# Performance work log

Measured on AMD Instinct MI355X. Metric: run time of the kernel, lower is better.

Reference implementation:

```python
import jax, jax.numpy as jnp
import numpy as np

T, H, I, E = 512, 2048, 1408, 16
G, TOPK_GROUP, TOP_K = 4, 2, 6
RSF = 2.5  # routed_scaling_factor


def setup_inputs() -> dict:
    key = jax.random.key(0)
    ks = jax.random.split(key, 6)
    s = jnp.float32(0.02)
    return {
        "hidden_states": jax.random.normal(ks[0], (T, H), jnp.float32),
        "gate_weight": jax.random.normal(ks[1], (E, H), jnp.float32) * s,
        "correction_bias": jax.random.normal(ks[2], (E,), jnp.float32) * s,
        "w_gate": jax.random.normal(ks[3], (E, I, H), jnp.float32) * s,
        "w_up": jax.random.normal(ks[4], (E, I, H), jnp.float32) * s,
        "w_down": jax.random.normal(ks[5], (E, H, I), jnp.float32) * s,
    }


def _route(x, gate_weight, correction_bias):
    # MoEGate: logits = x @ W^T ; noaux_tc biased grouped top-k (sigmoid scoring)
    logits = x @ gate_weight.T                       # [T, E]
    scores = jax.nn.sigmoid(logits)                  # [T, E]
    sfc = scores + correction_bias                   # scores used for selection only
    # group score = sum of top-2 biased scores within each group
    gs = sfc.reshape(-1, G, E // G)                  # [T, G, E/G]
    group_scores = jax.lax.top_k(gs, 2)[0].sum(-1)   # [T, G]
    gidx = jax.lax.top_k(group_scores, TOPK_GROUP)[1]        # [T, topk_group]
    gmask = jnp.sum(jax.nn.one_hot(gidx, G, dtype=x.dtype), axis=1)  # [T, G]
    emask = jnp.repeat(gmask, E // G, axis=1)        # [T, E]
    masked = jnp.where(emask > 0, sfc, -jnp.inf)
    topk_idx = jax.lax.top_k(masked, TOP_K)[1]       # [T, K]
    # weights come from the UNbiased sigmoid scores
    topk_w = jnp.take_along_axis(scores, topk_idx, axis=1)   # [T, K]
    topk_w = topk_w / jnp.sum(topk_w, axis=-1, keepdims=True)  # renormalize
    topk_w = topk_w * jnp.asarray(RSF, x.dtype)      # routed_scaling_factor
    return topk_w, topk_idx


def _moe(x, topk_w, topk_idx, w_gate, w_up, w_down):
    # dispatch/grouped-GEMM/combine, expressed as a scan over experts with
    # per-token combine coefficients (same math as gather/grouped-GEMM/scatter)
    def step(acc, ws):
        wg, wu, wd, e = ws
        h = jax.nn.silu(x @ wg.T) * (x @ wu.T)       # [T, I] SiluAndMul
        out_e = h @ wd.T                             # [T, H]
        coef = jnp.sum(jnp.where(topk_idx == e, topk_w, 0.0), axis=1)  # [T]
        return acc + coef[:, None] * out_e, None

    acc0 = jnp.zeros_like(x)
    acc, _ = jax.lax.scan(step, acc0, (w_gate, w_up, w_down, jnp.arange(E)))
    return acc


def reference(hidden_states, gate_weight, correction_bias, w_gate, w_up, w_down):
    topk_w, topk_idx = _route(hidden_states, gate_weight, correction_bias)
    return _moe(hidden_states, topk_w, topk_idx, w_gate, w_up, w_down)
```

## Files before the change

kernel.cpp:

```cpp
#include <hip/hip_runtime.h>
#include <cstdint>

#define T_TOK 512
#define H_DIM 2048
#define I_DIM 1408
#define N_EXP 16

typedef __attribute__((ext_vector_type(8))) _Float16 f16x8;
typedef __attribute__((ext_vector_type(4))) float f32x4;

__device__ __forceinline__ void gload_lds16(const void* g, void* l) {
  auto gp = (const __attribute__((address_space(1))) unsigned int*)(unsigned long long)g;
  unsigned int loff = (unsigned int)(unsigned long long)l;
  auto lp = (__attribute__((address_space(3))) unsigned int*)loff;
  __builtin_amdgcn_global_load_lds(gp, lp, 16, 0, 0);
}

__device__ __forceinline__ f16x8 cvt8(f32x4 a, f32x4 b) {
  f16x8 r;
  r[0] = (_Float16)a[0]; r[1] = (_Float16)a[1]; r[2] = (_Float16)a[2]; r[3] = (_Float16)a[3];
  r[4] = (_Float16)b[0]; r[5] = (_Float16)b[1]; r[6] = (_Float16)b[2]; r[7] = (_Float16)b[3];
  return r;
}

__global__ __launch_bounds__(256) void route_kernel(
    const float* __restrict__ x, const float* __restrict__ gw,
    const float* __restrict__ bias, float* __restrict__ coef,
    _Float16* __restrict__ xb) {
  const int t = blockIdx.x;
  const int tid = threadIdx.x;
  const float* xt = x + (size_t)t * H_DIM;
  _Float16* xbt = xb + (size_t)t * H_DIM;

  float part[N_EXP];
#pragma unroll
  for (int e = 0; e < N_EXP; ++e) part[e] = 0.f;
  for (int j = tid; j < H_DIM; j += 256) {
    float xv = xt[j];
    xbt[j] = (_Float16)xv;
#pragma unroll
    for (int e = 0; e < N_EXP; ++e) part[e] += xv * gw[e * H_DIM + j];
  }
#pragma unroll
  for (int e = 0; e < N_EXP; ++e) {
#pragma unroll
    for (int off = 32; off > 0; off >>= 1) part[e] += __shfl_down(part[e], off);
  }
  __shared__ float red[4][N_EXP];
  const int lane = tid & 63, w = tid >> 6;
  if (lane == 0) {
#pragma unroll
    for (int e = 0; e < N_EXP; ++e) red[w][e] = part[e];
  }
  __syncthreads();
  if (tid == 0) {
    float s[16], sf[16];
    for (int e = 0; e < 16; ++e) {
      float lg = red[0][e] + red[1][e] + red[2][e] + red[3][e];
      s[e] = 1.f / (1.f + expf(-lg));
      sf[e] = s[e] + bias[e];
    }
    float gsc[4];
    for (int g = 0; g < 4; ++g) {
      float m1 = -1e30f, m2 = -1e30f;
      for (int j = 0; j < 4; ++j) {
        float v = sf[g * 4 + j];
        if (v > m1) { m2 = m1; m1 = v; }
        else if (v > m2) { m2 = v; }
      }
      gsc[g] = m1 + m2;
    }
    int g1 = 0;
    for (int g = 1; g < 4; ++g) if (gsc[g] > gsc[g1]) g1 = g;
    int g2 = -1;
    for (int g = 0; g < 4; ++g) {
      if (g == g1) continue;
      if (g2 < 0 || gsc[g] > gsc[g2]) g2 = g;
    }
    bool gok[4];
    for (int g = 0; g < 4; ++g) gok[g] = (g == g1) || (g == g2);
    bool sel[16];
    for (int e = 0; e < 16; ++e) sel[e] = false;
    float wsum = 0.f;
    for (int k = 0; k < 6; ++k) {
      int best = -1; float bv = 0.f;
      for (int e2 = 0; e2 < 16; ++e2) {
        if (!gok[e2 >> 2] || sel[e2]) continue;
        if (best < 0 || sf[e2] > bv) { bv = sf[e2]; best = e2; }
      }
      sel[best] = true;
      wsum += s[best];
    }
    float inv = 2.5f / wsum;
    for (int e = 0; e < 16; ++e) coef[t * N_EXP + e] = sel[e] ? s[e] * inv : 0.f;
  }
}

__global__ __launch_bounds__(512) void build_lists_kernel(
    const float* __restrict__ coef, int* __restrict__ counts,
    int* __restrict__ lists) {
  const int e = blockIdx.x;
  const int t = threadIdx.x;
  const bool flag = coef[t * N_EXP + e] != 0.f;
  const unsigned long long m = __ballot(flag);
  const int lane = t & 63, w = t >> 6;
  __shared__ int wcnt[8], woff[8];
  if (lane == 0) wcnt[w] = __popcll(m);
  __syncthreads();
  if (t == 0) {
    int a = 0;
    for (int i = 0; i < 8; ++i) { woff[i] = a; a += wcnt[i]; }
    counts[e] = a;
  }
  __syncthreads();
  if (flag) {
    int pos = woff[w] + __popcll(m & ((1ull << lane) - 1ull));
    lists[e * T_TOK + pos] = t;
  }
}

__global__ __launch_bounds__(256, 2) void gate_up_kernel(
    const _Float16* __restrict__ xb, const float* __restrict__ wg,
    const float* __restrict__ wu, const int* __restrict__ counts,
    const int* __restrict__ lists, _Float16* __restrict__ hbuf) {
  extern __shared__ char lds[];
  const int e = blockIdx.z;
  const int ne = counts[e];
  const int row0 = blockIdx.y * 256;
  if (row0 >= ne) return;
  const int col0 = blockIdx.x * 64;
  const int tid = threadIdx.x;
  const int lane = tid & 63;
  const int w = tid >> 6;

  const int* lst = lists + e * T_TOK;
  const _Float16* asrc[4];
#pragma unroll
  for (int i = 0; i < 4; ++i) {
    int r = row0 + (4 * w + i) * 16 + (lane & 15);
    int tok = lst[min(r, ne - 1)];
    asrc[i] = xb + (size_t)tok * H_DIM + (lane >> 4) * 8;
  }
  const float* bgs[2];
  const float* bus[2];
#pragma unroll
  for (int i = 0; i < 2; ++i) {
    int tr = (w * 2 + i) * 8 + (lane >> 3);
    int ls = (lane & 7) ^ (tr & 7);
    bgs[i] = wg + ((size_t)e * I_DIM + col0 + tr) * H_DIM + ls * 4;
    bus[i] = wu + ((size_t)e * I_DIM + col0 + tr) * H_DIM + ls * 4;
  }

  f32x4 accg[4][4], accu[4][4];
  const f32x4 zz = {0.f, 0.f, 0.f, 0.f};
#pragma unroll
  for (int m = 0; m < 4; ++m)
#pragma unroll
    for (int n = 0; n < 4; ++n) { accg[m][n] = zz; accu[m][n] = zz; }

  auto stage = [&](int kt, int buf) {
    const int k0 = kt * 32;
#pragma unroll
    for (int i = 0; i < 4; ++i)
      gload_lds16(asrc[i] + k0, lds + buf * 16384 + (4 * w + i) * 1024);
#pragma unroll
    for (int i = 0; i < 2; ++i) {
      gload_lds16(bgs[i] + k0, lds + 32768 + buf * 8192 + (w * 2 + i) * 1024);
      gload_lds16(bus[i] + k0, lds + 49152 + buf * 8192 + (w * 2 + i) * 1024);
    }
  };

  auto comp = [&](int buf) {
    const char* Ab = lds + buf * 16384;
    const char* Gb = lds + 32768 + buf * 8192;
    const char* Ub = lds + 49152 + buf * 8192;
    f16x8 afr[4];
#pragma unroll
    for (int m = 0; m < 4; ++m)
      afr[m] = *(const f16x8*)(Ab + (w * 4 + m) * 1024 + lane * 16);
    const int s0 = (lane >> 4) * 2;
#pragma unroll
    for (int n = 0; n < 4; ++n) {
      int c = n * 16 + (lane & 15);
      int p0 = s0 ^ (c & 7);
      int p1 = (s0 + 1) ^ (c & 7);
      f16x8 bg = cvt8(*(const f32x4*)(Gb + c * 128 + p0 * 16),
                      *(const f32x4*)(Gb + c * 128 + p1 * 16));
      f16x8 bu = cvt8(*(const f32x4*)(Ub + c * 128 + p0 * 16),
                      *(const f32x4*)(Ub + c * 128 + p1 * 16));
#pragma unroll
      for (int m = 0; m < 4; ++m) {
        accg[m][n] = __builtin_amdgcn_mfma_f32_16x16x32_f16(afr[m], bg, accg[m][n], 0, 0, 0);
        accu[m][n] = __builtin_amdgcn_mfma_f32_16x16x32_f16(afr[m], bu, accu[m][n], 0, 0, 0);
      }
    }
  };

  const int NK = H_DIM / 32;
  stage(0, 0);
  for (int kt = 0; kt < NK; ++kt) {
    __syncthreads();
    if (kt + 1 < NK) stage(kt + 1, (kt + 1) & 1);
    comp(kt & 1);
  }

  _Float16* hb = hbuf + (size_t)e * T_TOK * I_DIM;
#pragma unroll
  for (int m = 0; m < 4; ++m) {
#pragma unroll
    for (int j = 0; j < 4; ++j) {
      int r = row0 + w * 64 + m * 16 + (lane >> 4) * 4 + j;
      if (r < ne) {
#pragma unroll
        for (int n = 0; n < 4; ++n) {
          int cc = col0 + n * 16 + (lane & 15);
          float g = accg[m][n][j];
          float u = accu[m][n][j];
          float hv = (g / (1.f + __expf(-g))) * u;
          hb[(size_t)r * I_DIM + cc] = (_Float16)hv;
        }
      }
    }
  }
}

__global__ __launch_bounds__(512) void down_kernel(
    const _Float16* __restrict__ hbuf, const float* __restrict__ wd,
    const int* __restrict__ counts, const int* __restrict__ lists,
    const float* __restrict__ coef, float* __restrict__ out) {
  extern __shared__ char lds[];
  const int e = blockIdx.z;
  const int ne = counts[e];
  const int row0 = blockIdx.y * 256;
  if (row0 >= ne) return;
  const int col0 = blockIdx.x * 64;
  const int tid = threadIdx.x;
  const int lane = tid & 63;
  const int w = tid >> 6;
  const int wr = w >> 1, wc = w & 1;

  const _Float16* hb = hbuf + (size_t)e * T_TOK * I_DIM;
  const _Float16* asrc[4];
#pragma unroll
  for (int i = 0; i < 4; ++i) {
    int tr = (w * 4 + i) * 8 + (lane >> 3);
    int lchunk = (lane & 7) ^ (tr & 7);
    asrc[i] = hb + (size_t)(row0 + tr) * I_DIM + lchunk * 8;
  }
  const float* bds[2];
#pragma unroll
  for (int i = 0; i < 2; ++i) {
    int tr = (w * 2 + i) * 4 + (lane >> 4);
    int ls = (lane & 15) ^ ((tr & 7) << 1);
    bds[i] = wd + ((size_t)e * H_DIM + col0 + tr) * I_DIM + ls * 4;
  }

  f32x4 acc[4][2];
  const f32x4 zz = {0.f, 0.f, 0.f, 0.f};
#pragma unroll
  for (int m = 0; m < 4; ++m)
#pragma unroll
    for (int n = 0; n < 2; ++n) acc[m][n] = zz;

  auto stage = [&](int kt, int buf) {
    const int k0 = kt * 64;
#pragma unroll
    for (int i = 0; i < 4; ++i)
      gload_lds16(asrc[i] + k0, lds + buf * 32768 + (w * 4 + i) * 1024);
#pragma unroll
    for (int i = 0; i < 2; ++i)
      gload_lds16(bds[i] + k0, lds + 65536 + buf * 16384 + (w * 2 + i) * 1024);
  };

  auto comp = [&](int buf) {
    const char* Ab = lds + buf * 32768;
    const char* Bb = lds + 65536 + buf * 16384;
#pragma unroll
    for (int kk = 0; kk < 2; ++kk) {
      f16x8 afr[4], bf[2];
#pragma unroll
      for (int m = 0; m < 4; ++m) {
        int row = wr * 64 + m * 16 + (lane & 15);
        int pch = (kk * 4 + (lane >> 4)) ^ (row & 7);
        afr[m] = *(const f16x8*)(Ab + row * 128 + pch * 16);
      }
#pragma unroll
      for (int n = 0; n < 2; ++n) {
        int c = wc * 32 + n * 16 + (lane & 15);
        int s0 = kk * 8 + (lane >> 4) * 2;
        int p0 = s0 ^ ((c & 7) << 1);
        int p1 = (s0 + 1) ^ ((c & 7) << 1);
        bf[n] = cvt8(*(const f32x4*)(Bb + c * 256 + p0 * 16),
                     *(const f32x4*)(Bb + c * 256 + p1 * 16));
      }
#pragma unroll
      for (int m = 0; m < 4; ++m)
#pragma unroll
        for (int n = 0; n < 2; ++n)
          acc[m][n] = __builtin_amdgcn_mfma_f32_16x16x32_f16(afr[m], bf[n], acc[m][n], 0, 0, 0);
    }
  };

  const int NK = I_DIM / 64;
  stage(0, 0);
  for (int kt = 0; kt < NK; ++kt) {
    __syncthreads();
    if (kt + 1 < NK) stage(kt + 1, (kt + 1) & 1);
    comp(kt & 1);
  }

#pragma unroll
  for (int m = 0; m < 4; ++m) {
#pragma unroll
    for (int j = 0; j < 4; ++j) {
      int r = row0 + wr * 64 + m * 16 + (lane >> 4) * 4 + j;
      if (r < ne) {
        int tok = lists[e * T_TOK + r];
        float c = coef[tok * N_EXP + e];
#pragma unroll
        for (int n = 0; n < 2; ++n) {
          int cc = col0 + wc * 32 + n * 16 + (lane & 15);
          atomicAdd(&out[(size_t)tok * H_DIM + cc], acc[m][n][j] * c);
        }
      }
    }
  }
}

extern "C" void kernel_launch(void* const* d_in, const int* in_sizes, int n_in,
                              void* d_out, int out_size, void* d_ws, size_t ws_size,
                              hipStream_t stream) {
  const float* x  = (const float*)d_in[0];
  const float* gw = (const float*)d_in[1];
  const float* cb = (const float*)d_in[2];
  const float* wg = (const float*)d_in[3];
  const float* wu = (const float*)d_in[4];
  const float* wd = (const float*)d_in[5];
  float* out = (float*)d_out;
  char* ws = (char*)d_ws;

  float* coef   = (float*)(ws);
  int*   counts = (int*)(ws + 32768);
  int*   lists  = (int*)(ws + 33024);
  _Float16* xb  = (_Float16*)(ws + 66048);
  _Float16* hbuf= (_Float16*)(ws + 66048 + 2097152 + 256);

  hipFuncSetAttribute((const void*)gate_up_kernel,
                      hipFuncAttributeMaxDynamicSharedMemorySize, 65536);
  hipFuncSetAttribute((const void*)down_kernel,
                      hipFuncAttributeMaxDynamicSharedMemorySize, 98304);

  hipMemsetAsync(d_out, 0, (size_t)out_size * sizeof(float), stream);

  route_kernel<<<T_TOK, 256, 0, stream>>>(x, gw, cb, coef, xb);
  build_lists_kernel<<<N_EXP, 512, 0, stream>>>(coef, counts, lists);
  gate_up_kernel<<<dim3(I_DIM / 64, 2, N_EXP), 256, 65536, stream>>>(xb, wg, wu, counts, lists, hbuf);
  down_kernel<<<dim3(H_DIM / 64, 2, N_EXP), 512, 98304, stream>>>(hbuf, wd, counts, lists, coef, out);
}
```

Measured before the change: 225.4 us.

## Narrow gate_up column tile to 32 and prefetch two K-stages ahead with vmcnt waits

The gate/up kernel's column tile drops from 64 to 32, doubling the number of blocks and halving the per-block weight staging and accumulator registers. LDS use falls to 48 KB, allocated statically. The K loop now issues loads two stages ahead and waits with a partial vmcnt instead of a full __syncthreads drain, so global-to-LDS loads overlap compute. The cost is twice the A-tile (token activation) loads across blocks, and correctness now depends on hand-counted vmcnt values and explicit barriers.

```diff
diff --git a/kernel.cpp b/kernel.cpp
--- a/kernel.cpp
+++ b/kernel.cpp
@@ -119,16 +119,16 @@
   }
 }
 
-__global__ __launch_bounds__(256, 2) void gate_up_kernel(
+__global__ __launch_bounds__(256) void gate_up_kernel(
     const _Float16* __restrict__ xb, const float* __restrict__ wg,
     const float* __restrict__ wu, const int* __restrict__ counts,
     const int* __restrict__ lists, _Float16* __restrict__ hbuf) {
-  extern __shared__ char lds[];
+  __shared__ char lds[49152];
   const int e = blockIdx.z;
   const int ne = counts[e];
   const int row0 = blockIdx.y * 256;
   if (row0 >= ne) return;
-  const int col0 = blockIdx.x * 64;
+  const int col0 = blockIdx.x * 32;
   const int tid = threadIdx.x;
   const int lane = tid & 63;
   const int w = tid >> 6;
@@ -141,46 +141,38 @@
     int tok = lst[min(r, ne - 1)];
     asrc[i] = xb + (size_t)tok * H_DIM + (lane >> 4) * 8;
   }
-  const float* bgs[2];
-  const float* bus[2];
-#pragma unroll
-  for (int i = 0; i < 2; ++i) {
-    int tr = (w * 2 + i) * 8 + (lane >> 3);
-    int ls = (lane & 7) ^ (tr & 7);
-    bgs[i] = wg + ((size_t)e * I_DIM + col0 + tr) * H_DIM + ls * 4;
-    bus[i] = wu + ((size_t)e * I_DIM + col0 + tr) * H_DIM + ls * 4;
-  }
-
-  f32x4 accg[4][4], accu[4][4];
+  const int btr = w * 8 + (lane >> 3);
+  const int bls = (lane & 7) ^ (btr & 7);
+  const float* bgsrc = wg + ((size_t)e * I_DIM + col0 + btr) * H_DIM + bls * 4;
+  const float* busrc = wu + ((size_t)e * I_DIM + col0 + btr) * H_DIM + bls * 4;
+
+  f32x4 accg[4][2], accu[4][2];
   const f32x4 zz = {0.f, 0.f, 0.f, 0.f};
 #pragma unroll
   for (int m = 0; m < 4; ++m)
 #pragma unroll
-    for (int n = 0; n < 4; ++n) { accg[m][n] = zz; accu[m][n] = zz; }
+    for (int n = 0; n < 2; ++n) { accg[m][n] = zz; accu[m][n] = zz; }
 
   auto stage = [&](int kt, int buf) {
     const int k0 = kt * 32;
 #pragma unroll
     for (int i = 0; i < 4; ++i)
       gload_lds16(asrc[i] + k0, lds + buf * 16384 + (4 * w + i) * 1024);
-#pragma unroll
-    for (int i = 0; i < 2; ++i) {
-      gload_lds16(bgs[i] + k0, lds + 32768 + buf * 8192 + (w * 2 + i) * 1024);
-      gload_lds16(bus[i] + k0, lds + 49152 + buf * 8192 + (w * 2 + i) * 1024);
-    }
+    gload_lds16(bgsrc + k0, lds + 32768 + buf * 4096 + w * 1024);
+    gload_lds16(busrc + k0, lds + 40960 + buf * 4096 + w * 1024);
   };
 
   auto comp = [&](int buf) {
     const char* Ab = lds + buf * 16384;
-    const char* Gb = lds + 32768 + buf * 8192;
-    const char* Ub = lds + 49152 + buf * 8192;
+    const char* Gb = lds + 32768 + buf * 4096;
+    const char* Ub = lds + 40960 + buf * 4096;
     f16x8 afr[4];
 #pragma unroll
     for (int m = 0; m < 4; ++m)
       afr[m] = *(const f16x8*)(Ab + (w * 4 + m) * 1024 + lane * 16);
     const int s0 = (lane >> 4) * 2;
 #pragma unroll
-    for (int n = 0; n < 4; ++n) {
+    for (int n = 0; n < 2; ++n) {
       int c = n * 16 + (lane & 15);
       int p0 = s0 ^ (c & 7);
       int p1 = (s0 + 1) ^ (c & 7);
@@ -198,10 +190,16 @@
 
   const int NK = H_DIM / 32;
   stage(0, 0);
+  stage(1, 1);
   for (int kt = 0; kt < NK; ++kt) {
-    __syncthreads();
-    if (kt + 1 < NK) stage(kt + 1, (kt + 1) & 1);
+    if (kt < NK - 1) { asm volatile("s_waitcnt vmcnt(6)" ::: "memory"); }
+    else             { asm volatile("s_waitcnt vmcnt(0)" ::: "memory"); }
+    __builtin_amdgcn_s_barrier();
+    asm volatile("" ::: "memory");
     comp(kt & 1);
+    asm volatile("" ::: "memory");
+    __builtin_amdgcn_s_barrier();
+    if (kt + 2 < NK) stage(kt + 2, kt & 1);
   }
 
   _Float16* hb = hbuf + (size_t)e * T_TOK * I_DIM;
@@ -212,7 +210,7 @@
       int r = row0 + w * 64 + m * 16 + (lane >> 4) * 4 + j;
       if (r < ne) {
 #pragma unroll
-        for (int n = 0; n < 4; ++n) {
+        for (int n = 0; n < 2; ++n) {
           int cc = col0 + n * 16 + (lane & 15);
           float g = accg[m][n][j];
           float u = accu[m][n][j];
@@ -345,8 +343,6 @@
   _Float16* xb  = (_Float16*)(ws + 66048);
   _Float16* hbuf= (_Float16*)(ws + 66048 + 2097152 + 256);
 
-  hipFuncSetAttribute((const void*)gate_up_kernel,
-                      hipFuncAttributeMaxDynamicSharedMemorySize, 65536);
   hipFuncSetAttribute((const void*)down_kernel,
                       hipFuncAttributeMaxDynamicSharedMemorySize, 98304);
 
@@ -354,6 +350,6 @@
 
   route_kernel<<<T_TOK, 256, 0, stream>>>(x, gw, cb, coef, xb);
   build_lists_kernel<<<N_EXP, 512, 0, stream>>>(coef, counts, lists);
-  gate_up_kernel<<<dim3(I_DIM / 64, 2, N_EXP), 256, 65536, stream>>>(xb, wg, wu, counts, lists, hbuf);
+  gate_up_kernel<<<dim3(I_DIM / 32, 2, N_EXP), 256, 0, stream>>>(xb, wg, wu, counts, lists, hbuf);
   down_kernel<<<dim3(H_DIM / 64, 2, N_EXP), 512, 98304, stream>>>(hbuf, wd, counts, lists, coef, out);
 }
```

After: 257.0 us. 14.0% more time.
